# Kernel optimization log

Hardware: AMD Instinct MI355X
Metric: run time of the kernel (lower is better)

Reference implementation:

```python
import jax, jax.numpy as jnp
import numpy as np

N_VARS = 100
MAX_LAG = 10
HIDDEN = 64
E = N_VARS * MAX_LAG  # number of tiny expert MLPs
BATCH = 4096


def setup_inputs() -> dict:
    key = jax.random.key(0)
    k_x, k_w1, k_b1, k_w2, k_b2 = jax.random.split(key, 5)
    x = jax.random.normal(k_x, (BATCH, E), dtype=jnp.float32)
    # PyTorch Linear(1, H): weight [H,1] -> stacked as [E, H]; bias [E, H]
    lim1 = 1.0  # kaiming-uniform-ish bound for fan_in=1
    W1 = jax.random.uniform(k_w1, (E, HIDDEN), dtype=jnp.float32, minval=-lim1, maxval=lim1)
    b1 = jax.random.uniform(k_b1, (E, HIDDEN), dtype=jnp.float32, minval=-lim1, maxval=lim1)
    # Linear(H, n_vars): weight [n_vars,H] -> stacked as [E, H, n_vars]; bias [E, n_vars]
    lim2 = 1.0 / np.sqrt(HIDDEN)
    W2 = jax.random.uniform(k_w2, (E, HIDDEN, N_VARS), dtype=jnp.float32, minval=-lim2, maxval=lim2)
    b2 = jax.random.uniform(k_b2, (E, N_VARS), dtype=jnp.float32, minval=-lim2, maxval=lim2)
    return {"x": x, "W1": W1, "b1": b1, "W2": W2, "b2": b2}


def reference(x, W1, b1, W2, b2):
    # Fused form of: sum_i Linear2_i(relu(Linear1_i(x[:, i:i+1])))
    # h[b,e,h] = relu(x[b,e] * W1[e,h] + b1[e,h])
    h = jax.nn.relu(x[:, :, None] * W1[None, :, :] + b1[None, :, :])  # [B,E,H]
    # sum over experts folded into the contraction: out[b,v] = sum_e h[b,e,:] @ W2[e,:,v]
    out = jnp.einsum("beh,ehv->bv", h, W2) + jnp.sum(b2, axis=0)  # [B,n_vars]
    return out
```

## Files before the change

kernel.cpp:

```cpp
#include <hip/hip_runtime.h>
#include <hip/hip_bf16.h>

#define NV 100
#define HID 64
#define NE 1000
#define NB 4096
#define ESPLIT 32
#define BLOBU 3584
#define NVP 112

typedef __attribute__((ext_vector_type(8))) short short8;
typedef __attribute__((ext_vector_type(8))) unsigned short ushort8;
typedef __attribute__((ext_vector_type(4))) float f32x4;
typedef __attribute__((ext_vector_type(2))) float f32x2;
typedef __attribute__((ext_vector_type(4))) unsigned u32x4;
typedef __attribute__((ext_vector_type(4))) unsigned short u16x4;

__device__ __align__(16) float g_bsum[NV];

__device__ __forceinline__ unsigned short f2bf(float f) {
    return (unsigned short)__builtin_bit_cast(short, (__bf16)f);
}
__device__ __forceinline__ short cvtbf(float f) {
    return __builtin_bit_cast(short, (__bf16)f);
}
__device__ __forceinline__ float bf2f(unsigned short s) {
    union { unsigned u; float f; } v; v.u = ((unsigned)s) << 16;
    return v.f;
}
__device__ __forceinline__ unsigned pkbf(float a, float b) {
    return (unsigned)f2bf(a) | ((unsigned)f2bf(b) << 16);
}

__device__ __forceinline__ unsigned pk_h(f32x2 xx, f32x2 w, f32x2 b, unsigned zero) {
    f32x2 d;
    asm("v_pk_fma_f32 %0, %1, %2, %3" : "=v"(d) : "v"(xx), "v"(w), "v"(b));
    unsigned u;
    asm("v_cvt_pk_bf16_f32 %0, %1, %2" : "=v"(u) : "v"(d.x), "v"(d.y));
    asm("v_pk_max_i16 %0, %1, %2" : "=v"(u) : "v"(u), "v"(zero));
    return u;
}

__device__ __host__ __forceinline__ void esplit_range(int ks, int* pe0, int* pne) {
    int e0 = (ks < 26) ? 32 * ks : 832 + 28 * (ks - 26);
    int ne = (ks < 26) ? 32 : 28;
    *pe0 = e0; *pne = ne;
}

__global__ void bias_kernel(const float* __restrict__ b2) {
    int v = blockIdx.x;
    float s = 0.f;
    for (int e = threadIdx.x; e < NE; e += 256)
        s += b2[e * NV + v];
    __shared__ float red[4];
    for (int off = 32; off; off >>= 1) s += __shfl_down(s, off, 64);
    if ((threadIdx.x & 63) == 0) red[threadIdx.x >> 6] = s;
    __syncthreads();
    if (threadIdx.x == 0) g_bsum[v] = red[0] + red[1] + red[2] + red[3];
}

__global__ void init_kernel(float* __restrict__ out) {
    int idx = blockIdx.x * 256 + threadIdx.x;
    if (idx < NB * NV) out[idx] = g_bsum[idx % NV];
}

__global__ void prepass7(const float* __restrict__ W2, unsigned* __restrict__ blob) {
    __shared__ float t[HID][NV + 1];
    int e = blockIdx.x;
    const float* src = W2 + (size_t)e * (HID * NV);
    for (int i = threadIdx.x; i < HID * NV; i += 256) {
        int hh = i / NV;
        int v = i - hh * NV;
        t[hh][v] = src[i];
    }
    __syncthreads();
    unsigned* dst = blob + (size_t)e * BLOBU;
    for (int o = threadIdx.x; o < BLOBU; o += 256) {
        int f = o >> 8;
        int r = o & 255;
        int l = r >> 2;
        int q = r & 3;
        int ksh = f / 7, tt = f - 7 * ksh;
        int kg = l >> 4, lrow = l & 15;
        int h0 = ksh * 32 + kg * 8 + 2 * q;
        int v = tt * 16 + lrow;
        unsigned val = 0;
        if (v < NV) val = pkbf(t[h0][v], t[h0 + 1][v]);
        dst[o] = val;
    }
}

__global__ __launch_bounds__(256, 2) void moe15(
    const float* __restrict__ x, const float* __restrict__ W1,
    const float* __restrict__ b1, const unsigned* __restrict__ blob,
    unsigned short* __restrict__ part)
{
    __shared__ __align__(16) unsigned short xts[32 * 256];
    __shared__ __align__(16) float w1l[32 * 64];
    __shared__ __align__(16) float b1l[32 * 64];

    const int bid = blockIdx.x;
    const int xcd = bid & 7;
    const int jj  = bid >> 3;
    const int ks  = xcd * 4 + (jj & 3);
    const int mb  = jj >> 2;

    const int tid  = threadIdx.x;
    const int lane = tid & 63;
    const int wave = tid >> 6;
    const int lrow = lane & 15;
    const int kg   = lane >> 4;

    const int row0 = mb * 256;
    int e0, ne; esplit_range(ks, &e0, &ne);

    {
        int r = tid;
        int slot = (r >> 6) * 64 + (r & 15) * 4 + ((r >> 4) & 3);
        const float* xp = x + (size_t)(row0 + r) * NE + e0;
        #pragma unroll
        for (int c4 = 0; c4 < 8; ++c4) {
            int eb = c4 * 4;
            if (eb < ne) {
                float4 v = *(const float4*)(xp + eb);
                xts[(eb + 0) * 256 + slot] = f2bf(v.x);
                xts[(eb + 1) * 256 + slot] = f2bf(v.y);
                xts[(eb + 2) * 256 + slot] = f2bf(v.z);
                xts[(eb + 3) * 256 + slot] = f2bf(v.w);
            }
        }
    }
    {
        int e = tid >> 3;
        int h = (tid & 7) * 8;
        if (e < ne) {
            const float* wsrc = W1 + (size_t)(e0 + e) * HID + h;
            const float* bsrc = b1 + (size_t)(e0 + e) * HID + h;
            *(float4*)&w1l[e * 64 + h]     = *(const float4*)(wsrc);
            *(float4*)&w1l[e * 64 + h + 4] = *(const float4*)(wsrc + 4);
            *(float4*)&b1l[e * 64 + h]     = *(const float4*)(bsrc);
            *(float4*)&b1l[e * 64 + h + 4] = *(const float4*)(bsrc + 4);
        }
    }
    __syncthreads();

    f32x4 acc[4][7];
    #pragma unroll
    for (int rf = 0; rf < 4; ++rf)
        #pragma unroll
        for (int t = 0; t < 7; ++t)
            acc[rf][t] = (f32x4){0.f, 0.f, 0.f, 0.f};

    u32x4 B0[7], B1[7];
    const int boff = lane * 4;

    auto LOADS0 = [&](const unsigned* g) {
        #pragma unroll
        for (int t = 0; t < 7; ++t)
            B0[t] = *(const u32x4*)(g + t * 256 + boff);
    };
    auto LOADS1 = [&](const unsigned* g) {
        #pragma unroll
        for (int t = 0; t < 7; ++t)
            B1[t] = *(const u32x4*)(g + (7 + t) * 256 + boff);
    };

    unsigned zero = 0;

    float4 Wc[4];
    auto WLOAD = [&](int e, int ksh) {
        const int hb = ksh * 32 + kg * 8;
        Wc[0] = *(const float4*)&w1l[e * 64 + hb];
        Wc[1] = *(const float4*)&w1l[e * 64 + hb + 4];
        Wc[2] = *(const float4*)&b1l[e * 64 + hb];
        Wc[3] = *(const float4*)&b1l[e * 64 + hb + 4];
    };

    auto BUILD = [&](short8* afr, const float* xv) {
        const f32x2* wp = (const f32x2*)&Wc[0];
        #pragma unroll
        for (int rf = 0; rf < 4; ++rf) {
            f32x2 xx = {xv[rf], xv[rf]};
            unsigned* au = (unsigned*)&afr[rf];
            au[0] = pk_h(xx, wp[0], wp[4], zero);
            au[1] = pk_h(xx, wp[1], wp[5], zero);
            au[2] = pk_h(xx, wp[2], wp[6], zero);
            au[3] = pk_h(xx, wp[3], wp[7], zero);
        }
    };

    const unsigned* gcur = blob + (size_t)e0 * BLOBU;
    LOADS0(gcur);
    LOADS1(gcur);

    const unsigned short* xrow = &xts[wave * 64 + lrow * 4];

    short8 afr0[4], afr1[4];
    float xvC[4], xvN[4];
    {
        u16x4 xq = *(const u16x4*)xrow;
        #pragma unroll
        for (int rf = 0; rf < 4; ++rf) xvC[rf] = bf2f(xq[rf]);
    }
    WLOAD(0, 0);

    for (int ei = 0; ei < ne; ++ei) {
        const int en = (ei + 1 < ne) ? ei + 1 : ei;
        const unsigned* gnext = blob + (size_t)(e0 + en) * BLOBU;

        BUILD(afr0, xvC);
        WLOAD(ei, 1);
        BUILD(afr1, xvC);
        {
            u16x4 xq = *(const u16x4*)(xrow + en * 256);
            #pragma unroll
            for (int rf = 0; rf < 4; ++rf) xvN[rf] = bf2f(xq[rf]);
        }

        __builtin_amdgcn_s_setprio(1);
        #pragma unroll
        for (int t = 0; t < 7; ++t) {
            short8 bf = __builtin_bit_cast(short8, B0[t]);
            #pragma unroll
            for (int rf = 0; rf < 4; ++rf)
                acc[rf][t] = __builtin_amdgcn_mfma_f32_16x16x32_bf16(afr0[rf], bf, acc[rf][t], 0, 0, 0);
        }
        #pragma unroll
        for (int t = 0; t < 7; ++t) {
            short8 bf = __builtin_bit_cast(short8, B1[t]);
            #pragma unroll
            for (int rf = 0; rf < 4; ++rf)
                acc[rf][t] = __builtin_amdgcn_mfma_f32_16x16x32_bf16(afr1[rf], bf, acc[rf][t], 0, 0, 0);
        }
        __builtin_amdgcn_s_setprio(0);

        LOADS0(gnext);
        LOADS1(gnext);
        WLOAD(en, 0);
        #pragma unroll
        for (int rf = 0; rf < 4; ++rf) xvC[rf] = xvN[rf];
    }

    unsigned short* dst = part + (size_t)ks * (NB * NVP);
    #pragma unroll
    for (int rf = 0; rf < 4; ++rf) {
        #pragma unroll
        for (int t = 0; t < 7; ++t) {
            int col = t * 16 + lrow;
            size_t base = (size_t)(row0 + wave * 64 + rf * 16 + kg * 4) * NVP + col;
            #pragma unroll
            for (int r = 0; r < 4; ++r)
                dst[base + (size_t)r * NVP] = (unsigned short)cvtbf(acc[rf][t][r]);
        }
    }
}

__global__ void reduce3(const unsigned short* __restrict__ part, float* __restrict__ out) {
    int idx = blockIdx.x * 256 + threadIdx.x;
    if (idx >= NB * (NVP / 8)) return;
    int b = idx / (NVP / 8);
    int g = idx - b * (NVP / 8);
    int c0 = g * 8;
    float s[8];
    #pragma unroll
    for (int j = 0; j < 8; ++j)
        s[j] = (c0 + j < NV) ? g_bsum[c0 + j] : 0.f;
    size_t off = (size_t)b * NVP + c0;
    #pragma unroll 4
    for (int k = 0; k < ESPLIT; ++k) {
        ushort8 v = *(const ushort8*)&part[(size_t)k * (NB * NVP) + off];
        #pragma unroll
        for (int j = 0; j < 8; ++j)
            s[j] += bf2f(v[j]);
    }
    #pragma unroll
    for (int j = 0; j < 8; ++j)
        if (c0 + j < NV) out[(size_t)b * NV + c0 + j] = s[j];
}

#define LDW 72
__global__ __launch_bounds__(256, 3) void moe_fallback(
    const float* __restrict__ x, const float* __restrict__ W1,
    const float* __restrict__ b1, const float* __restrict__ W2,
    float* __restrict__ dst)
{
    __shared__ unsigned short w2t[8192];
    const int tid  = threadIdx.x;
    const int lane = tid & 63;
    const int lrow = lane & 15;
    const int kg   = lane >> 4;
    const int wave = tid >> 6;
    const int row0 = blockIdx.x * 128 + wave * 32;
    const int e0 = blockIdx.y * 32;
    const int e1 = min(NE, e0 + 32);

    f32x4 acc[2][7];
    #pragma unroll
    for (int rf = 0; rf < 2; ++rf)
        #pragma unroll
        for (int t = 0; t < 7; ++t)
            acc[rf][t] = (f32x4){0.f, 0.f, 0.f, 0.f};

    const float* xr0 = x + (size_t)(row0 + lrow) * NE;
    const float* xr1 = x + (size_t)(row0 + 16 + lrow) * NE;

    for (int e = e0; e < e1; ++e) {
        __syncthreads();
        const float* src = W2 + (size_t)e * (HID * NV);
        unsigned* w2t32 = (unsigned*)w2t;
        #pragma unroll
        for (int k = 0; k < 13; ++k) {
            int i = tid + k * 256;
            if (i < (HID / 2) * NV) {
                int a3  = i / 400;
                int rem = i - a3 * 400;
                int bv  = rem >> 2;
                int c   = rem & 3;
                int hh2 = a3 * 4 + c;
                float f0 = src[(2 * hh2) * NV + bv];
                float f1 = src[(2 * hh2 + 1) * NV + bv];
                w2t32[bv * (LDW / 2) + hh2] = pkbf(f0, f1);
            }
        }
        __syncthreads();

        float xv0 = xr0[e];
        float xv1 = xr1[e];
        const float* w1p = W1 + e * HID;
        const float* b1p = b1 + e * HID;
        #pragma unroll
        for (int ksh = 0; ksh < 2; ++ksh) {
            const int hb = ksh * 32 + kg * 8;
            f32x4 w1lo = *(const f32x4*)(w1p + hb);
            f32x4 w1hi = *(const f32x4*)(w1p + hb + 4);
            f32x4 blo  = *(const f32x4*)(b1p + hb);
            f32x4 bhi  = *(const f32x4*)(b1p + hb + 4);
            short8 a0, a1;
            #pragma unroll
            for (int j = 0; j < 4; ++j) {
                a0[j]     = cvtbf(fmaxf(fmaf(xv0, w1lo[j], blo[j]), 0.f));
                a0[j + 4] = cvtbf(fmaxf(fmaf(xv0, w1hi[j], bhi[j]), 0.f));
                a1[j]     = cvtbf(fmaxf(fmaf(xv1, w1lo[j], blo[j]), 0.f));
                a1[j + 4] = cvtbf(fmaxf(fmaf(xv1, w1hi[j], bhi[j]), 0.f));
            }
            #pragma unroll
            for (int t = 0; t < 7; ++t) {
                short8 bf = *(const short8*)&w2t[(t * 16 + lrow) * LDW + hb];
                acc[0][t] = __builtin_amdgcn_mfma_f32_16x16x32_bf16(a0, bf, acc[0][t], 0, 0, 0);
                acc[1][t] = __builtin_amdgcn_mfma_f32_16x16x32_bf16(a1, bf, acc[1][t], 0, 0, 0);
            }
        }
    }

    #pragma unroll
    for (int rf = 0; rf < 2; ++rf) {
        #pragma unroll
        for (int t = 0; t < 7; ++t) {
            int col = t * 16 + lrow;
            if (col < NV) {
                size_t base = (size_t)(row0 + rf * 16 + kg * 4) * NV + col;
                #pragma unroll
                for (int r = 0; r < 4; ++r)
                    atomicAdd(&dst[base + (size_t)r * NV], acc[rf][t][r]);
            }
        }
    }
}

extern "C" void kernel_launch(void* const* d_in, const int* in_sizes, int n_in,
                              void* d_out, int out_size, void* d_ws, size_t ws_size,
                              hipStream_t stream) {
    const float* x  = (const float*)d_in[0];
    const float* W1 = (const float*)d_in[1];
    const float* b1 = (const float*)d_in[2];
    const float* W2 = (const float*)d_in[3];
    const float* b2 = (const float*)d_in[4];
    float* out = (float*)d_out;

    const size_t BLOB_BYTES = (size_t)NE * BLOBU * 4;
    const size_t PART_BYTES = (size_t)ESPLIT * NB * NVP * 2;

    bias_kernel<<<NV, 256, 0, stream>>>(b2);

    if (ws_size >= BLOB_BYTES + PART_BYTES) {
        unsigned* blob = (unsigned*)d_ws;
        unsigned short* part = (unsigned short*)((char*)d_ws + BLOB_BYTES);
        prepass7<<<NE, 256, 0, stream>>>(W2, blob);
        moe15<<<512, 256, 0, stream>>>(x, W1, b1, blob, part);
        reduce3<<<(NB * (NVP / 8) + 255) / 256, 256, 0, stream>>>(part, out);
    } else {
        init_kernel<<<(NB * NV + 255) / 256, 256, 0, stream>>>(out);
        moe_fallback<<<dim3(NB / 128, ESPLIT), 256, 0, stream>>>(x, W1, b1, W2, out);
    }
}
```

Baseline: 79.91 us.

## Stage expert W2 blobs into LDS via async global_load_lds double buffering

The main MoE kernel stops loading each expert's packed W2 fragments straight from global memory into registers. It now double-buffers them in LDS with async global-to-LDS loads, and all waves read the B fragments from shared memory. The row tile is halved to 128 rows per block, with twice as many blocks and a higher occupancy target (3 blocks per CU), which cuts accumulator registers. In exchange it adds a block-wide barrier per expert and reads W2 from L2 twice as many times across the grid.

```diff
diff --git a/kernel.cpp b/kernel.cpp
--- a/kernel.cpp
+++ b/kernel.cpp
@@ -8,13 +8,13 @@
 #define ESPLIT 32
 #define BLOBU 3584
 #define NVP 112
+#define EXPB 14336
 
 typedef __attribute__((ext_vector_type(8))) short short8;
 typedef __attribute__((ext_vector_type(8))) unsigned short ushort8;
 typedef __attribute__((ext_vector_type(4))) float f32x4;
 typedef __attribute__((ext_vector_type(2))) float f32x2;
 typedef __attribute__((ext_vector_type(4))) unsigned u32x4;
-typedef __attribute__((ext_vector_type(4))) unsigned short u16x4;
 
 __device__ __align__(16) float g_bsum[NV];
 
@@ -90,14 +90,15 @@
     }
 }
 
-__global__ __launch_bounds__(256, 2) void moe15(
+__global__ __launch_bounds__(256, 3) void moe17(
     const float* __restrict__ x, const float* __restrict__ W1,
     const float* __restrict__ b1, const unsigned* __restrict__ blob,
     unsigned short* __restrict__ part)
 {
-    __shared__ __align__(16) unsigned short xts[32 * 256];
-    __shared__ __align__(16) float w1l[32 * 64];
-    __shared__ __align__(16) float b1l[32 * 64];
+    __shared__ __align__(16) unsigned char smem[53248];
+    unsigned short* xts = (unsigned short*)(smem + 28672);
+    float* w1l = (float*)(smem + 36864);
+    float* b1l = (float*)(smem + 45056);
 
     const int bid = blockIdx.x;
     const int xcd = bid & 7;
@@ -111,22 +112,22 @@
     const int lrow = lane & 15;
     const int kg   = lane >> 4;
 
-    const int row0 = mb * 256;
+    const int row0 = mb * 128;
     int e0, ne; esplit_range(ks, &e0, &ne);
 
     {
-        int r = tid;
-        int slot = (r >> 6) * 64 + (r & 15) * 4 + ((r >> 4) & 3);
+        int r = tid & 127, half = tid >> 7;
+        int slot = (r >> 5) * 32 + (r & 15) * 2 + ((r >> 4) & 1);
         const float* xp = x + (size_t)(row0 + r) * NE + e0;
         #pragma unroll
-        for (int c4 = 0; c4 < 8; ++c4) {
-            int eb = c4 * 4;
+        for (int c4 = 0; c4 < 4; ++c4) {
+            int eb = half * 16 + c4 * 4;
             if (eb < ne) {
                 float4 v = *(const float4*)(xp + eb);
-                xts[(eb + 0) * 256 + slot] = f2bf(v.x);
-                xts[(eb + 1) * 256 + slot] = f2bf(v.y);
-                xts[(eb + 2) * 256 + slot] = f2bf(v.z);
-                xts[(eb + 3) * 256 + slot] = f2bf(v.w);
+                xts[(eb + 0) * 128 + slot] = f2bf(v.x);
+                xts[(eb + 1) * 128 + slot] = f2bf(v.y);
+                xts[(eb + 2) * 128 + slot] = f2bf(v.z);
+                xts[(eb + 3) * 128 + slot] = f2bf(v.w);
             }
         }
     }
@@ -142,112 +143,82 @@
             *(float4*)&b1l[e * 64 + h + 4] = *(const float4*)(bsrc + 4);
         }
     }
+
+    auto stage = [&](int buf, int e) {
+        const unsigned* g = blob + (size_t)e * BLOBU;
+        unsigned* lbase = (unsigned*)(smem + buf * EXPB);
+        #pragma unroll
+        for (int k = 0; k < 3; ++k) {
+            int off = (k * 256 + tid) * 4;
+            __builtin_amdgcn_global_load_lds(
+                (const __attribute__((address_space(1))) unsigned*)(g + off),
+                (__attribute__((address_space(3))) unsigned*)(lbase + off),
+                16, 0, 0);
+        }
+        if (tid < 128) {
+            int off = (768 + tid) * 4;
+            __builtin_amdgcn_global_load_lds(
+                (const __attribute__((address_space(1))) unsigned*)(g + off),
+                (__attribute__((address_space(3))) unsigned*)(lbase + off),
+                16, 0, 0);
+        }
+    };
+
+    stage(0, e0);
     __syncthreads();
 
-    f32x4 acc[4][7];
-    #pragma unroll
-    for (int rf = 0; rf < 4; ++rf)
+    f32x4 acc[2][7];
+    #pragma unroll
+    for (int rf = 0; rf < 2; ++rf)
         #pragma unroll
         for (int t = 0; t < 7; ++t)
             acc[rf][t] = (f32x4){0.f, 0.f, 0.f, 0.f};
 
-    u32x4 B0[7], B1[7];
-    const int boff = lane * 4;
-
-    auto LOADS0 = [&](const unsigned* g) {
-        #pragma unroll
-        for (int t = 0; t < 7; ++t)
-            B0[t] = *(const u32x4*)(g + t * 256 + boff);
-    };
-    auto LOADS1 = [&](const unsigned* g) {
-        #pragma unroll
-        for (int t = 0; t < 7; ++t)
-            B1[t] = *(const u32x4*)(g + (7 + t) * 256 + boff);
-    };
-
     unsigned zero = 0;
-
-    float4 Wc[4];
-    auto WLOAD = [&](int e, int ksh) {
-        const int hb = ksh * 32 + kg * 8;
-        Wc[0] = *(const float4*)&w1l[e * 64 + hb];
-        Wc[1] = *(const float4*)&w1l[e * 64 + hb + 4];
-        Wc[2] = *(const float4*)&b1l[e * 64 + hb];
-        Wc[3] = *(const float4*)&b1l[e * 64 + hb + 4];
-    };
-
-    auto BUILD = [&](short8* afr, const float* xv) {
-        const f32x2* wp = (const f32x2*)&Wc[0];
-        #pragma unroll
-        for (int rf = 0; rf < 4; ++rf) {
-            f32x2 xx = {xv[rf], xv[rf]};
-            unsigned* au = (unsigned*)&afr[rf];
-            au[0] = pk_h(xx, wp[0], wp[4], zero);
-            au[1] = pk_h(xx, wp[1], wp[5], zero);
-            au[2] = pk_h(xx, wp[2], wp[6], zero);
-            au[3] = pk_h(xx, wp[3], wp[7], zero);
-        }
-    };
-
-    const unsigned* gcur = blob + (size_t)e0 * BLOBU;
-    LOADS0(gcur);
-    LOADS1(gcur);
-
-    const unsigned short* xrow = &xts[wave * 64 + lrow * 4];
-
-    short8 afr0[4], afr1[4];
-    float xvC[4], xvN[4];
-    {
-        u16x4 xq = *(const u16x4*)xrow;
-        #pragma unroll
-        for (int rf = 0; rf < 4; ++rf) xvC[rf] = bf2f(xq[rf]);
-    }
-    WLOAD(0, 0);
-
+    int cur = 0;
     for (int ei = 0; ei < ne; ++ei) {
-        const int en = (ei + 1 < ne) ? ei + 1 : ei;
-        const unsigned* gnext = blob + (size_t)(e0 + en) * BLOBU;
-
-        BUILD(afr0, xvC);
-        WLOAD(ei, 1);
-        BUILD(afr1, xvC);
-        {
-            u16x4 xq = *(const u16x4*)(xrow + en * 256);
-            #pragma unroll
-            for (int rf = 0; rf < 4; ++rf) xvN[rf] = bf2f(xq[rf]);
-        }
-
-        __builtin_amdgcn_s_setprio(1);
-        #pragma unroll
-        for (int t = 0; t < 7; ++t) {
-            short8 bf = __builtin_bit_cast(short8, B0[t]);
-            #pragma unroll
-            for (int rf = 0; rf < 4; ++rf)
-                acc[rf][t] = __builtin_amdgcn_mfma_f32_16x16x32_bf16(afr0[rf], bf, acc[rf][t], 0, 0, 0);
-        }
-        #pragma unroll
-        for (int t = 0; t < 7; ++t) {
-            short8 bf = __builtin_bit_cast(short8, B1[t]);
-            #pragma unroll
-            for (int rf = 0; rf < 4; ++rf)
-                acc[rf][t] = __builtin_amdgcn_mfma_f32_16x16x32_bf16(afr1[rf], bf, acc[rf][t], 0, 0, 0);
-        }
-        __builtin_amdgcn_s_setprio(0);
-
-        LOADS0(gnext);
-        LOADS1(gnext);
-        WLOAD(en, 0);
-        #pragma unroll
-        for (int rf = 0; rf < 4; ++rf) xvC[rf] = xvN[rf];
+        if (ei + 1 < ne) stage(cur ^ 1, e0 + ei + 1);
+
+        const unsigned char* bufc = smem + cur * EXPB;
+        unsigned xw = *(const unsigned*)&xts[ei * 128 + wave * 32 + lrow * 2];
+        f32x2 xx0 = {bf2f((unsigned short)(xw & 0xffffu)), bf2f((unsigned short)(xw & 0xffffu))};
+        f32x2 xx1 = {bf2f((unsigned short)(xw >> 16)),     bf2f((unsigned short)(xw >> 16))};
+
+        #pragma unroll
+        for (int ksh = 0; ksh < 2; ++ksh) {
+            const int hb = ksh * 32 + kg * 8;
+            const f32x2* wp = (const f32x2*)&w1l[ei * 64 + hb];
+            const f32x2* bp = (const f32x2*)&b1l[ei * 64 + hb];
+
+            short8 a0, a1;
+            unsigned* a0u = (unsigned*)&a0;
+            unsigned* a1u = (unsigned*)&a1;
+            #pragma unroll
+            for (int q = 0; q < 4; ++q) {
+                a0u[q] = pk_h(xx0, wp[q], bp[q], zero);
+                a1u[q] = pk_h(xx1, wp[q], bp[q], zero);
+            }
+
+            __builtin_amdgcn_s_setprio(1);
+            #pragma unroll
+            for (int t = 0; t < 7; ++t) {
+                short8 bf = *(const short8*)(bufc + ((ksh * 7 + t) << 10) + lane * 16);
+                acc[0][t] = __builtin_amdgcn_mfma_f32_16x16x32_bf16(a0, bf, acc[0][t], 0, 0, 0);
+                acc[1][t] = __builtin_amdgcn_mfma_f32_16x16x32_bf16(a1, bf, acc[1][t], 0, 0, 0);
+            }
+            __builtin_amdgcn_s_setprio(0);
+        }
+        __syncthreads();
+        cur ^= 1;
     }
 
     unsigned short* dst = part + (size_t)ks * (NB * NVP);
     #pragma unroll
-    for (int rf = 0; rf < 4; ++rf) {
+    for (int rf = 0; rf < 2; ++rf) {
         #pragma unroll
         for (int t = 0; t < 7; ++t) {
             int col = t * 16 + lrow;
-            size_t base = (size_t)(row0 + wave * 64 + rf * 16 + kg * 4) * NVP + col;
+            size_t base = (size_t)(row0 + wave * 32 + rf * 16 + kg * 4) * NVP + col;
             #pragma unroll
             for (int r = 0; r < 4; ++r)
                 dst[base + (size_t)r * NVP] = (unsigned short)cvtbf(acc[rf][t][r]);
@@ -386,7 +357,7 @@
         unsigned* blob = (unsigned*)d_ws;
         unsigned short* part = (unsigned short*)((char*)d_ws + BLOB_BYTES);
         prepass7<<<NE, 256, 0, stream>>>(W2, blob);
-        moe15<<<512, 256, 0, stream>>>(x, W1, b1, blob, part);
+        moe17<<<1024, 256, 0, stream>>>(x, W1, b1, blob, part);
         reduce3<<<(NB * (NVP / 8) + 255) / 256, 256, 0, stream>>>(part, out);
     } else {
         init_kernel<<<(NB * NV + 255) / 256, 256, 0, stream>>>(out);
```

Result: slower. 93.22 us (+16.7%).
